# Optimization experiments

Hardware: AMD Instinct MI355X
Metric: run time of the kernel (lower is better)

The kernel has to match this reference:

```python
import jax, jax.numpy as jnp
import numpy as np

EMBED_DIM = 1024
NUM_HEADS = 16
N_POS = 2048
BATCH = 4


def setup_inputs() -> dict:
    key = jax.random.key(0)
    k_x, k_w1, k_b1, k_wo, k_bo = jax.random.split(key, 5)
    s1 = 1.0 / np.sqrt(EMBED_DIM)
    x = jax.random.normal(k_x, (BATCH, N_POS, EMBED_DIM), dtype=jnp.float32)
    # torch Linear weights stored as [in, out] for x @ W + b
    W_qkv = jax.random.uniform(k_w1, (EMBED_DIM, 3 * EMBED_DIM), dtype=jnp.float32, minval=-s1, maxval=s1)
    b_qkv = jax.random.uniform(k_b1, (3 * EMBED_DIM,), dtype=jnp.float32, minval=-s1, maxval=s1)
    W_o = jax.random.uniform(k_wo, (EMBED_DIM, EMBED_DIM), dtype=jnp.float32, minval=-s1, maxval=s1)
    b_o = jax.random.uniform(k_bo, (EMBED_DIM,), dtype=jnp.float32, minval=-s1, maxval=s1)
    return {"x": x, "W_qkv": W_qkv, "b_qkv": b_qkv, "W_o": W_o, "b_o": b_o}


def reference(x, W_qkv, b_qkv, W_o, b_o):
    B, N, C = x.shape
    H = NUM_HEADS
    d_k = C // H
    qkv = x @ W_qkv + b_qkv                       # [B, N, 3C]
    q, k, v = jnp.split(qkv, 3, axis=-1)
    q = q.reshape(B, N, H, d_k).transpose(0, 2, 1, 3)  # [B, H, N, d_k]
    k = k.reshape(B, N, H, d_k).transpose(0, 2, 1, 3)
    v = v.reshape(B, N, H, d_k).transpose(0, 2, 1, 3)
    scores = jnp.einsum('bhqd,bhkd->bhqk', q, k) * (1.0 / np.sqrt(d_k))
    causal = jnp.tril(jnp.ones((N, N), dtype=bool))
    scores = jnp.where(causal, scores, -jnp.inf)
    attn = jax.nn.softmax(scores, axis=-1)
    out = jnp.einsum('bhqk,bhkd->bhqd', attn, v)  # [B, H, N, d_k]
    out = out.transpose(0, 2, 1, 3).reshape(B, N, C)
    return out @ W_o + b_o
```

## Files before the change

kernel.cpp:

```cpp
#include <hip/hip_runtime.h>
#include <hip/hip_bf16.h>

typedef __attribute__((ext_vector_type(8))) __bf16 bf16x8;
typedef __attribute__((ext_vector_type(4))) float f32x4;
typedef __attribute__((ext_vector_type(16))) float f32x16;
typedef __attribute__((ext_vector_type(4))) unsigned short u16x4;
typedef __attribute__((ext_vector_type(8))) unsigned short u16x8;
typedef __attribute__((ext_vector_type(4))) unsigned int u32x4;
typedef unsigned short u16;

#define MFMA16 __builtin_amdgcn_mfma_f32_16x16x32_bf16
#define MFMA32 __builtin_amdgcn_mfma_f32_32x32x16_bf16

#if __has_builtin(__builtin_amdgcn_exp2f)
#define EXP2F __builtin_amdgcn_exp2f
#else
#define EXP2F(x) __expf((x) * 0.69314718056f)
#endif

__device__ inline u16 f32_to_bf16_bits(float f) {
    unsigned u = __builtin_bit_cast(unsigned, f);
    unsigned r = u + 0x7FFFu + ((u >> 16) & 1u);
    return (u16)(r >> 16);
}

__device__ inline void g2l16(const void* g, void* l) {
    __builtin_amdgcn_global_load_lds(
        (const __attribute__((address_space(1))) unsigned int*)g,
        (__attribute__((address_space(3))) unsigned int*)l,
        16, 0, 0);
}

__device__ inline float red32_max(float x) { return fmaxf(x, __shfl_xor(x, 32)); }
__device__ inline float red32_sum(float x) { return x + __shfl_xor(x, 32); }

__global__ void cvt_bf16_kernel(const float* __restrict__ in, u16* __restrict__ out, int n) {
    int i = (blockIdx.x * 256 + threadIdx.x) * 4;
    if (i >= n) return;
    f32x4 v = *(const f32x4*)&in[i];
    u16x4 r;
#pragma unroll
    for (int j = 0; j < 4; ++j) r[j] = f32_to_bf16_bits(v[j]);
    *(u16x4*)&out[i] = r;
}

__global__ __launch_bounds__(256) void cvt_t_kernel(const float* __restrict__ W,
                                                    u16* __restrict__ WT, int K, int N) {
    const int w = threadIdx.x >> 6, l = threadIdx.x & 63;
    const int n = blockIdx.x * 64 + l;
    const int k0 = blockIdx.y * 32 + w * 8;
    u16x8 r;
#pragma unroll
    for (int i = 0; i < 8; ++i)
        r[i] = f32_to_bf16_bits(W[(size_t)(k0 + i) * N + n]);
    *(u16x8*)&WT[(size_t)n * K + k0] = r;
}

template <int STORE_BF16>
__global__ __launch_bounds__(256) void gemm_nt(
    const u16* __restrict__ A, const u16* __restrict__ BT,
    const float* __restrict__ bias, void* __restrict__ Cv,
    int M, int N, int K, int qcols, float qscale, int nbx)
{
    __shared__ __align__(16) u16 SM[24576];
    const int tid = threadIdx.x;
    const int w = tid >> 6, l = tid & 63;
    const int lr = l & 15, lh = l >> 4;
    const int wr = (w >> 1) * 64, wc = (w & 1) * 64;

    const int nwg = gridDim.x;
    const int swz = (blockIdx.x & 7) * (nwg >> 3) + (blockIdx.x >> 3);
    const int m0 = (swz / nbx) * 128;
    const int n0 = (swz % nbx) * 128;

    const int NT = K >> 5;

    const int f0 = tid, f1 = 256 + tid;
    const int r0 = f0 >> 2, r1 = f1 >> 2;
    const int cs0 = ((f0 & 3) ^ ((r0 >> 1) & 3)) * 8;
    const int cs1 = ((f1 & 3) ^ ((r1 >> 1) & 3)) * 8;
    const size_t arow0 = (size_t)(m0 + r0) * K, arow1 = (size_t)(m0 + r1) * K;
    const size_t brow0 = (size_t)(n0 + r0) * K, brow1 = (size_t)(n0 + r1) * K;

#define STAGE_TILE(t, set)                                                     \
    do {                                                                       \
        const int kk_ = (t) * 32;                                              \
        u16* dst_ = SM + (set) * 8192 + w * 512;                               \
        g2l16(A + arow0 + kk_ + cs0, dst_);                                    \
        g2l16(BT + brow0 + kk_ + cs0, dst_ + 4096);                            \
        g2l16(A + arow1 + kk_ + cs1, dst_ + 2048);                             \
        g2l16(BT + brow1 + kk_ + cs1, dst_ + 4096 + 2048);                     \
    } while (0)

    f32x4 acc[4][4];
#pragma unroll
    for (int m = 0; m < 4; ++m)
#pragma unroll
        for (int n = 0; n < 4; ++n) acc[m][n] = (f32x4)(0.0f);

    STAGE_TILE(0, 0);
    STAGE_TILE(1, 1);
    asm volatile("s_waitcnt vmcnt(4) lgkmcnt(0)\n\ts_barrier" ::: "memory");

    const int csw = (lr >> 1) & 3;
    int s0 = 0, s2 = 2;
    for (int t = 0; t < NT; ++t) {
        if (t + 2 < NT) STAGE_TILE(t + 2, s2);

        const u16* As = SM + s0 * 8192;
        const u16* Bs = As + 4096;
        bf16x8 af[4], bfr[4];
#pragma unroll
        for (int m = 0; m < 4; ++m)
            af[m] = *(const bf16x8*)&As[(wr + m * 16 + lr) * 32 + ((lh ^ csw) << 3)];
#pragma unroll
        for (int n = 0; n < 4; ++n)
            bfr[n] = *(const bf16x8*)&Bs[(wc + n * 16 + lr) * 32 + ((lh ^ csw) << 3)];
        __builtin_amdgcn_s_setprio(1);
#pragma unroll
        for (int m = 0; m < 4; ++m)
#pragma unroll
            for (int n = 0; n < 4; ++n)
                acc[m][n] = MFMA16(af[m], bfr[n], acc[m][n], 0, 0, 0);
        __builtin_amdgcn_s_setprio(0);

        if (t + 2 < NT)
            asm volatile("s_waitcnt vmcnt(4) lgkmcnt(0)\n\ts_barrier" ::: "memory");
        else if (t + 1 < NT)
            asm volatile("s_waitcnt vmcnt(0) lgkmcnt(0)\n\ts_barrier" ::: "memory");

        s0 = (s0 == 2) ? 0 : s0 + 1;
        s2 = (s2 == 2) ? 0 : s2 + 1;
    }
#undef STAGE_TILE

#pragma unroll
    for (int m = 0; m < 4; ++m) {
        int row = m0 + wr + m * 16 + lh * 4;
#pragma unroll
        for (int n = 0; n < 4; ++n) {
            int col = n0 + wc + n * 16 + lr;
            float bs = bias[col];
            float sc = (col < qcols) ? qscale : 1.0f;
#pragma unroll
            for (int j = 0; j < 4; ++j) {
                float v = (acc[m][n][j] + bs) * sc;
                if (STORE_BF16)
                    ((u16*)Cv)[(size_t)(row + j) * N + col] = f32_to_bf16_bits(v);
                else
                    ((float*)Cv)[(size_t)(row + j) * N + col] = v;
            }
        }
    }
}

__global__ __launch_bounds__(512, 2) void attn_kernel(
    const u16* __restrict__ qkv, u16* __restrict__ ctx)
{
    __shared__ __align__(16) u16 SM[17408];

    const int bid = blockIdx.x;
    const int xcd = bid & 7, jj = bid >> 3;
    const int bh = xcd * 8 + (jj >> 2);
    const int pr = jj & 3;
    const int b = bh >> 4, h = bh & 15;
    const size_t rowbase = (size_t)b * 2048;
    const int tid = threadIdx.x, w = tid >> 6, l = tid & 63;
    const int lq = l & 31, lk = l >> 5;

    const int rstage = w * 8 + (l >> 3);
    const int cstage = l & 7;
    const int kchunk = cstage ^ (l >> 3);

    bf16x8 vreg;

#pragma unroll
    for (int pass = 0; pass < 2; ++pass) {
        const int qt = pass ? (7 - pr) : pr;
        const int q0 = qt * 256;
        const int nt = 4 * qt + 4;
        const int qbase = q0 + w * 32;

        const u16* qp = qkv + (rowbase + qbase + lq) * 3072 + h * 64 + lk * 8;
        bf16x8 qf[4];
#pragma unroll
        for (int j = 0; j < 4; ++j) qf[j] = *(const bf16x8*)(qp + j * 16);

        f32x16 ot[2];
#pragma unroll
        for (int dt = 0; dt < 2; ++dt) ot[dt] = (f32x16)(0.0f);
        float m_run = -3e38f, l_run = 0.0f;

        __syncthreads();
        g2l16(qkv + (rowbase + rstage) * 3072 + 1024 + h * 64 + kchunk * 8, SM + w * 512);
        vreg = *(const bf16x8*)(qkv + (rowbase + rstage) * 3072 + 2048 + h * 64 + cstage * 8);
        asm volatile("s_waitcnt vmcnt(0)" ::: "memory");
#pragma unroll
        for (int i = 0; i < 8; ++i) {
            const int d = cstage * 8 + i;
            SM[8192 + (((d * 64 + rstage) ^ (((i ^ cstage) & 7) << 3)))] = ((const u16*)&vreg)[i];
        }
        __syncthreads();

        for (int t = 0; t < nt; ++t) {
            const int c = t & 1;
            const int kb = t * 64;
            u16* const Kb = SM + (c ? 4096 : 0);
            u16* const Vb = SM + 8192 + (c ? 4096 : 0);

            if (t + 1 < nt) {
                const int kb2 = kb + 64;
                g2l16(qkv + (rowbase + kb2 + rstage) * 3072 + 1024 + h * 64 + kchunk * 8,
                      SM + (c ? 0 : 4096) + w * 512);
                vreg = *(const bf16x8*)(qkv + (rowbase + kb2 + rstage) * 3072 + 2048 + h * 64 + cstage * 8);
            }

            if (kb <= qbase + 31) {
                bf16x8 kf[2][4];
#pragma unroll
                for (int kt = 0; kt < 2; ++kt)
#pragma unroll
                    for (int j = 0; j < 4; ++j)
                        kf[kt][j] = *(const bf16x8*)&Kb[((kt * 32 + lq) * 64 + j * 16 + lk * 8) ^ ((lq & 7) << 3)];

                f32x16 sf[2];
                __builtin_amdgcn_s_setprio(1);
#pragma unroll
                for (int kt = 0; kt < 2; ++kt) {
                    f32x16 z = (f32x16)(0.0f);
#pragma unroll
                    for (int j = 0; j < 4; ++j) z = MFMA32(kf[kt][j], qf[j], z, 0, 0, 0);
                    sf[kt] = z;
                }
                __builtin_amdgcn_s_setprio(0);

                float mt = -3e38f;
                if (kb + 63 > qbase) {
                    const int qrow = qbase + lq;
#pragma unroll
                    for (int kt = 0; kt < 2; ++kt)
#pragma unroll
                        for (int r = 0; r < 16; ++r) {
                            const int key = kb + kt * 32 + (r & 3) + 8 * (r >> 2) + 4 * lk;
                            float v = sf[kt][r];
                            if (key > qrow) v = -3e38f;
                            sf[kt][r] = v;
                            mt = fmaxf(mt, v);
                        }
                } else {
#pragma unroll
                    for (int kt = 0; kt < 2; ++kt)
#pragma unroll
                        for (int r = 0; r < 16; ++r) mt = fmaxf(mt, sf[kt][r]);
                }
                mt = red32_max(mt);

                const bool defer = __all(mt <= m_run + 16.0f);
                float mn = m_run;
                if (!defer) {
                    mn = fmaxf(m_run, mt);
                    const float alpha = EXP2F(m_run - mn);
                    m_run = mn;
                    l_run *= alpha;
#pragma unroll
                    for (int dt = 0; dt < 2; ++dt)
#pragma unroll
                        for (int r = 0; r < 16; ++r) ot[dt][r] *= alpha;
                }
                float rs = 0.0f;
#pragma unroll
                for (int kt = 0; kt < 2; ++kt)
#pragma unroll
                    for (int r = 0; r < 16; ++r) {
                        const float pp = EXP2F(sf[kt][r] - mn);
                        sf[kt][r] = pp;
                        rs += pp;
                    }
                l_run += red32_sum(rs);

                unsigned pc[2][4][2];
#pragma unroll
                for (int kt = 0; kt < 2; ++kt)
#pragma unroll
                    for (int rg = 0; rg < 4; ++rg) {
                        unsigned d0, d1;
                        asm("v_cvt_pk_bf16_f32 %0, %1, %2"
                            : "=v"(d0) : "v"((float)sf[kt][rg * 4 + 0]), "v"((float)sf[kt][rg * 4 + 1]));
                        asm("v_cvt_pk_bf16_f32 %0, %1, %2"
                            : "=v"(d1) : "v"((float)sf[kt][rg * 4 + 2]), "v"((float)sf[kt][rg * 4 + 3]));
                        pc[kt][rg][0] = d0;
                        pc[kt][rg][1] = d1;
                    }

                __builtin_amdgcn_s_setprio(1);
#pragma unroll
                for (int kt = 0; kt < 2; ++kt)
#pragma unroll
                    for (int hh = 0; hh < 2; ++hh) {
                        unsigned a0 = pc[kt][2 * hh][0], a1 = pc[kt][2 * hh][1];
                        unsigned b0 = pc[kt][2 * hh + 1][0], b1 = pc[kt][2 * hh + 1][1];
                        asm("v_permlane32_swap_b32 %0, %1" : "+v"(a0), "+v"(b0));
                        asm("v_permlane32_swap_b32 %0, %1" : "+v"(a1), "+v"(b1));
                        u32x4 wv = {a0, a1, b0, b1};
                        const bf16x8 pb = __builtin_bit_cast(bf16x8, wv);
                        const int k0 = 2 * kt + hh;
#pragma unroll
                        for (int dt = 0; dt < 2; ++dt) {
                            const int d = dt * 32 + lq;
                            const int vswz = ((d & 7) ^ (d >> 3)) & 7;
                            const bf16x8 vf = *(const bf16x8*)&Vb[((d * 64) + (k0 * 16 + lk * 8)) ^ (vswz << 3)];
                            ot[dt] = MFMA32(vf, pb, ot[dt], 0, 0, 0);
                        }
                    }
                __builtin_amdgcn_s_setprio(0);
            }

            asm volatile("s_waitcnt vmcnt(0)" ::: "memory");
            if (t + 1 < nt) {
                u16* const Vn = SM + 8192 + (c ? 0 : 4096);
#pragma unroll
                for (int i = 0; i < 8; ++i) {
                    const int d = cstage * 8 + i;
                    Vn[((d * 64 + rstage) ^ (((i ^ cstage) & 7) << 3))] = ((const u16*)&vreg)[i];
                }
            }
            __syncthreads();
        }

        u16* const out_l = SM + w * 2176;
        const float inv = 1.0f / l_run;
#pragma unroll
        for (int dt = 0; dt < 2; ++dt)
#pragma unroll
            for (int r = 0; r < 16; ++r) {
                const int d = dt * 32 + (r & 3) + 8 * (r >> 2) + 4 * lk;
                out_l[lq * 68 + d] = f32_to_bf16_bits(ot[dt][r] * inv);
            }
#pragma unroll
        for (int rr = 0; rr < 4; ++rr) {
            const int row = rr * 8 + (l >> 3);
            const bf16x8 v = *(const bf16x8*)&out_l[row * 68 + (l & 7) * 8];
            *(bf16x8*)(ctx + (rowbase + qbase + row) * 1024 + h * 64 + (l & 7) * 8) = v;
        }
    }
}

extern "C" void kernel_launch(void* const* d_in, const int* in_sizes, int n_in,
                              void* d_out, int out_size, void* d_ws, size_t ws_size,
                              hipStream_t stream) {
    const float* x      = (const float*)d_in[0];
    const float* W_qkv  = (const float*)d_in[1];
    const float* b_qkv  = (const float*)d_in[2];
    const float* W_o    = (const float*)d_in[3];
    const float* b_o    = (const float*)d_in[4];
    float* out = (float*)d_out;

    const int M = 4 * 2048;
    const int C = 1024;
    u16* qkv   = (u16*)d_ws;
    u16* xb    = qkv   + (size_t)M * 3 * C;
    u16* wqkvt = xb    + (size_t)M * C;
    u16* ctx   = wqkvt + (size_t)3 * C * C;
    u16* wot   = ctx   + (size_t)M * C;

    const float SCQ = 0.125f * 1.44269504089f;

    cvt_bf16_kernel<<<(M * C) / (256 * 4), 256, 0, stream>>>(x, xb, M * C);
    cvt_t_kernel<<<dim3(3 * C / 64, C / 32), 256, 0, stream>>>(W_qkv, wqkvt, C, 3 * C);
    cvt_t_kernel<<<dim3(C / 64, C / 32), 256, 0, stream>>>(W_o, wot, C, C);

    gemm_nt<1><<<(3 * C / 128) * (M / 128), 256, 0, stream>>>(xb, wqkvt, b_qkv, qkv,
                                                              M, 3 * C, C, C, SCQ, 3 * C / 128);

    attn_kernel<<<256, 512, 0, stream>>>(qkv, ctx);

    gemm_nt<0><<<(C / 128) * (M / 128), 256, 0, stream>>>(ctx, wot, b_o, out,
                                                          M, C, C, 0, 1.0f, C / 128);
}
```

Baseline: 169.1 us.

## Use 128x256 tiled GEMM with triple-buffered LDS for QKV projection

Adds a new GEMM kernel for the QKV projection. It uses 128x256 output tiles, with each wave computing 64x128 via 4x8 MFMA 16x16 tiles, and a three-stage LDS pipeline that prefetches two k-tiles ahead. The larger tile and deeper prefetch aim to increase data reuse per LDS load and hide global memory latency. In exchange it uses more LDS and accumulator registers, which may lower occupancy, and it launches half as many workgroups.

```diff
diff --git a/kernel.cpp b/kernel.cpp
--- a/kernel.cpp
+++ b/kernel.cpp
@@ -54,6 +54,115 @@
     for (int i = 0; i < 8; ++i)
         r[i] = f32_to_bf16_bits(W[(size_t)(k0 + i) * N + n]);
     *(u16x8*)&WT[(size_t)n * K + k0] = r;
+}
+
+template <int STORE_BF16>
+__global__ __launch_bounds__(256) void gemm_nt3(
+    const u16* __restrict__ A, const u16* __restrict__ BT,
+    const float* __restrict__ bias, void* __restrict__ Cv,
+    int M, int N, int K, int qcols, float qscale, int nbx)
+{
+    __shared__ __align__(16) u16 SM[36864];
+    const int tid = threadIdx.x;
+    const int w = tid >> 6, l = tid & 63;
+    const int lr = l & 15, lh = l >> 4;
+    const int wr = (w >> 1) * 64;
+    const int wc = (w & 1) * 128;
+
+    const int nwg = gridDim.x;
+    const int swz = (blockIdx.x & 7) * (nwg >> 3) + (blockIdx.x >> 3);
+    const int m0 = (swz / nbx) * 128;
+    const int n0 = (swz % nbx) * 256;
+
+    const int NT = K >> 5;
+
+    const int fa0 = tid, fa1 = 256 + tid;
+    const int ra0 = fa0 >> 2, ra1 = fa1 >> 2;
+    const int ca0 = ((fa0 & 3) ^ ((ra0 >> 1) & 3)) * 8;
+    const int ca1 = ((fa1 & 3) ^ ((ra1 >> 1) & 3)) * 8;
+    const size_t arow0 = (size_t)(m0 + ra0) * K, arow1 = (size_t)(m0 + ra1) * K;
+    int rb[4], cb[4];
+    size_t brow[4];
+#pragma unroll
+    for (int p = 0; p < 4; ++p) {
+        const int f = p * 256 + tid;
+        rb[p] = f >> 2;
+        cb[p] = ((f & 3) ^ ((rb[p] >> 1) & 3)) * 8;
+        brow[p] = (size_t)(n0 + rb[p]) * K;
+    }
+
+#define STAGE3(t, set)                                                         \
+    do {                                                                       \
+        const int kk_ = (t) * 32;                                              \
+        u16* dst_ = SM + (set) * 12288 + w * 512;                              \
+        g2l16(A + arow0 + kk_ + ca0, dst_);                                    \
+        g2l16(A + arow1 + kk_ + ca1, dst_ + 2048);                             \
+        g2l16(BT + brow[0] + kk_ + cb[0], dst_ + 4096);                        \
+        g2l16(BT + brow[1] + kk_ + cb[1], dst_ + 6144);                        \
+        g2l16(BT + brow[2] + kk_ + cb[2], dst_ + 8192);                        \
+        g2l16(BT + brow[3] + kk_ + cb[3], dst_ + 10240);                       \
+    } while (0)
+
+    f32x4 acc[4][8];
+#pragma unroll
+    for (int m = 0; m < 4; ++m)
+#pragma unroll
+        for (int n = 0; n < 8; ++n) acc[m][n] = (f32x4)(0.0f);
+
+    STAGE3(0, 0);
+    STAGE3(1, 1);
+    asm volatile("s_waitcnt vmcnt(6) lgkmcnt(0)\n\ts_barrier" ::: "memory");
+
+    const int csw = (lr >> 1) & 3;
+    int s0 = 0, s2 = 2;
+    for (int t = 0; t < NT; ++t) {
+        if (t + 2 < NT) STAGE3(t + 2, s2);
+
+        const u16* As = SM + s0 * 12288;
+        const u16* Bs = As + 4096;
+        bf16x8 af[4], bfr[8];
+#pragma unroll
+        for (int m = 0; m < 4; ++m)
+            af[m] = *(const bf16x8*)&As[(wr + m * 16 + lr) * 32 + ((lh ^ csw) << 3)];
+#pragma unroll
+        for (int n = 0; n < 8; ++n)
+            bfr[n] = *(const bf16x8*)&Bs[(wc + n * 16 + lr) * 32 + ((lh ^ csw) << 3)];
+        __builtin_amdgcn_s_setprio(1);
+#pragma unroll
+        for (int m = 0; m < 4; ++m)
+#pragma unroll
+            for (int n = 0; n < 8; ++n)
+                acc[m][n] = MFMA16(af[m], bfr[n], acc[m][n], 0, 0, 0);
+        __builtin_amdgcn_s_setprio(0);
+
+        if (t + 2 < NT)
+            asm volatile("s_waitcnt vmcnt(6) lgkmcnt(0)\n\ts_barrier" ::: "memory");
+        else if (t + 1 < NT)
+            asm volatile("s_waitcnt vmcnt(0) lgkmcnt(0)\n\ts_barrier" ::: "memory");
+
+        s0 = (s0 == 2) ? 0 : s0 + 1;
+        s2 = (s2 == 2) ? 0 : s2 + 1;
+    }
+#undef STAGE3
+
+#pragma unroll
+    for (int m = 0; m < 4; ++m) {
+        int row = m0 + wr + m * 16 + lh * 4;
+#pragma unroll
+        for (int n = 0; n < 8; ++n) {
+            int col = n0 + wc + n * 16 + lr;
+            float bs = bias[col];
+            float sc = (col < qcols) ? qscale : 1.0f;
+#pragma unroll
+            for (int j = 0; j < 4; ++j) {
+                float v = (acc[m][n][j] + bs) * sc;
+                if (STORE_BF16)
+                    ((u16*)Cv)[(size_t)(row + j) * N + col] = f32_to_bf16_bits(v);
+                else
+                    ((float*)Cv)[(size_t)(row + j) * N + col] = v;
+            }
+        }
+    }
 }
 
 template <int STORE_BF16>
@@ -369,8 +478,8 @@
     cvt_t_kernel<<<dim3(3 * C / 64, C / 32), 256, 0, stream>>>(W_qkv, wqkvt, C, 3 * C);
     cvt_t_kernel<<<dim3(C / 64, C / 32), 256, 0, stream>>>(W_o, wot, C, C);
 
-    gemm_nt<1><<<(3 * C / 128) * (M / 128), 256, 0, stream>>>(xb, wqkvt, b_qkv, qkv,
-                                                              M, 3 * C, C, C, SCQ, 3 * C / 128);
+    gemm_nt3<1><<<(M / 128) * (3 * C / 256), 256, 0, stream>>>(xb, wqkvt, b_qkv, qkv,
+                                                               M, 3 * C, C, C, SCQ, 3 * C / 256);
 
     attn_kernel<<<256, 512, 0, stream>>>(qkv, ctx);
 
```

After: 181.6 us. 1.07x slower.
